# Optimization experiments

Measured on AMD Instinct MI355X. Metric: run time of the kernel, lower is better.

The kernel has to match this reference:

```python
import jax, jax.numpy as jnp
import numpy as np

D_MODEL = 1024
N_HEADS = 16
D_HEAD = 64


def setup_inputs() -> dict:
    key = jax.random.key(0)
    ks = jax.random.split(key, 9)
    B, T = 2, 2048
    s_in = 1.0 / np.sqrt(D_MODEL)
    s_o = 1.0 / np.sqrt(N_HEADS * D_HEAD)
    return {
        "x": jax.random.normal(ks[0], (B, T, D_MODEL), dtype=jnp.float32),
        "wq": jax.random.normal(ks[1], (D_MODEL, N_HEADS * D_HEAD), dtype=jnp.float32) * s_in,
        "bq": jax.random.normal(ks[2], (N_HEADS * D_HEAD,), dtype=jnp.float32) * 0.01,
        "wk": jax.random.normal(ks[3], (D_MODEL, N_HEADS * D_HEAD), dtype=jnp.float32) * s_in,
        "bk": jax.random.normal(ks[4], (N_HEADS * D_HEAD,), dtype=jnp.float32) * 0.01,
        "wv": jax.random.normal(ks[5], (D_MODEL, N_HEADS * D_HEAD), dtype=jnp.float32) * s_in,
        "bv": jax.random.normal(ks[6], (N_HEADS * D_HEAD,), dtype=jnp.float32) * 0.01,
        "wo": jax.random.normal(ks[7], (N_HEADS * D_HEAD, D_MODEL), dtype=jnp.float32) * s_o,
        "bo": jax.random.normal(ks[8], (D_MODEL,), dtype=jnp.float32) * 0.01,
    }


def reference(x, wq, bq, wk, bk, wv, bv, wo, bo):
    B, T, _ = x.shape
    H, Dh = N_HEADS, D_HEAD
    # projections -> [B, H, T, Dh]
    q = (x @ wq + bq).reshape(B, T, H, Dh).transpose(0, 2, 1, 3)
    k = (x @ wk + bk).reshape(B, T, H, Dh).transpose(0, 2, 1, 3)
    v = (x @ wv + bv).reshape(B, T, H, Dh).transpose(0, 2, 1, 3)
    scale = 1.0 / np.sqrt(Dh).astype(np.float32)
    attn = jnp.einsum("bhqd,bhkd->bhqk", q, k) * scale  # [B,H,T,T]
    causal = jnp.tril(jnp.ones((T, T), dtype=bool))
    attn = jnp.where(causal, attn, jnp.float32(-jnp.inf))
    attn = jax.nn.softmax(attn, axis=-1)
    out = jnp.einsum("bhqk,bhkd->bhqd", attn, v)  # [B,H,T,Dh]
    out = out.transpose(0, 2, 1, 3).reshape(B, T, H * Dh)
    return out @ wo + bo
```

## Files before the change

kernel.cpp:

```cpp
#include <hip/hip_runtime.h>
#include <math.h>

#define D_MODEL 1024
#define N_HEADS 16
#define D_HEAD  64
#define B_SZ    2
#define T_SEQ   2048

typedef short bf16x8 __attribute__((ext_vector_type(8)));
typedef short bf16x4 __attribute__((ext_vector_type(4)));
typedef float f32x4  __attribute__((ext_vector_type(4)));
typedef unsigned short us4 __attribute__((ext_vector_type(4)));

__device__ __forceinline__ unsigned short f2bf(float f) {
  union { float f; unsigned u; } v; v.f = f;
  unsigned r = v.u + 0x7FFFu + ((v.u >> 16) & 1u);
  return (unsigned short)(r >> 16);
}
__device__ __forceinline__ float bf2f(unsigned short s) {
  union { unsigned u; float f; } v; v.u = ((unsigned)s) << 16;
  return v.f;
}
__device__ __forceinline__ unsigned pack2_rtz(float lo, float hi) {
  union { float f; unsigned u; } a, b; a.f = hi; b.f = lo;
  return __builtin_amdgcn_perm(a.u, b.u, 0x07060302u);
}

__device__ __forceinline__ void async_copy16(const unsigned short* g, unsigned short* l) {
  __builtin_amdgcn_global_load_lds(
      (__attribute__((address_space(1))) void*)(g),
      (__attribute__((address_space(3))) void*)(l), 16, 0, 0);
}

__device__ __forceinline__ unsigned short* opart_ptr(
    unsigned short* wtd, unsigned short* xbd, int p) {
  const size_t off = (size_t)p * 2048;
  const size_t RA  = (size_t)3 * 1024 * 1024;
  return (off < RA) ? (wtd + off) : (xbd + (off - RA));
}

__global__ __launch_bounds__(256) void conv_all(
    const float* __restrict__ x,
    const float* __restrict__ wq, const float* __restrict__ wk,
    const float* __restrict__ wv, const float* __restrict__ wo,
    unsigned short* __restrict__ wt, unsigned short* __restrict__ xb)
{
  const int z = blockIdx.z;
  if (z < 4) {
    const float* W = (z == 0) ? wq : (z == 1) ? wk : (z == 2) ? wv : wo;
    unsigned short* O = wt + (size_t)z * D_MODEL * D_MODEL;
    __shared__ float t[32][33];
    const int tx = threadIdx.x & 31, ty = threadIdx.x >> 5;
    const int kb = blockIdx.x * 32, nb = blockIdx.y * 32;
    #pragma unroll
    for (int i = 0; i < 4; i++)
      t[ty + i * 8][tx] = W[(size_t)(kb + ty + i * 8) * D_MODEL + nb + tx];
    __syncthreads();
    #pragma unroll
    for (int i = 0; i < 4; i++)
      O[(size_t)(nb + ty + i * 8) * D_MODEL + kb + tx] = f2bf(t[tx][ty + i * 8]);
  } else {
    const int row = (z - 4) * 1024 + blockIdx.y * 32 + (threadIdx.x >> 3);
    const int col = blockIdx.x * 32 + (threadIdx.x & 7) * 4;
    float4 v = *(const float4*)&x[(size_t)row * D_MODEL + col];
    us4 o = { f2bf(v.x), f2bf(v.y), f2bf(v.z), f2bf(v.w) };
    *(us4*)&xb[(size_t)row * D_MODEL + col] = o;
  }
}

#define BKg 64
#define NTg (D_MODEL / BKg)
#define QSCALE 0.180336879f

__global__ __launch_bounds__(256) void qkv_gemm(
    const unsigned short* __restrict__ A, const unsigned short* __restrict__ Bt,
    const float* __restrict__ bq, const float* __restrict__ bk,
    const float* __restrict__ bv, unsigned short* __restrict__ qkv,
    unsigned short* __restrict__ vT)
{
  __shared__ unsigned short As[2][128 * BKg];

  const int tid  = threadIdx.x;
  const int wv   = tid >> 6;
  const int lane = tid & 63;
  const int lr   = lane & 15;
  const int quad = lane >> 4;
  const int wm   = wv >> 1;
  const int wn   = wv & 1;
  const int row0 = blockIdx.x * 128;
  const int col0 = blockIdx.y * 64;
  const int K = D_MODEL;

  const int mid = col0 >> 10;
  const float* bias = (mid == 0) ? bq : (mid == 1) ? bk : bv;

  f32x4 acc[8];
  #pragma unroll
  for (int i = 0; i < 8; i++) acc[i] = (f32x4){0.f, 0.f, 0.f, 0.f};

  auto stageA = [&](int buf, int k0) {
    #pragma unroll
    for (int it = 0; it < 4; it++) {
      const int gg = wv * 256 + it * 64 + lane;
      const int r  = gg >> 3;
      const int gc = ((gg & 7) ^ (r & 7)) * 8;
      async_copy16(A + (size_t)(row0 + r) * K + k0 + gc,
                   &As[buf][(size_t)(wv * 256 + it * 64) * 8]);
    }
  };

  const int wsel = (mid == 2) ? wn : wm;
  const unsigned short* Wp = Bt + (size_t)(col0 + wsel * 32 + lr) * K + quad * 8;

  auto loadW = [&](int k0, bf16x8 W[2][2]) {
    #pragma unroll
    for (int mi = 0; mi < 2; mi++)
      #pragma unroll
      for (int hf = 0; hf < 2; hf++)
        W[mi][hf] = *(const bf16x8*)&Wp[(size_t)mi * 16 * K + k0 + hf * 32];
  };

  bf16x8 Wc[2][2], Wn[2][2];
  loadW(0, Wc);
  stageA(0, 0);
  int cur = 0;

  const int xrow = (mid == 2) ? wm : wn;

  for (int t = 0; t < NTg; ++t) {
    __syncthreads();

    bf16x8 xF[4][2];
    #pragma unroll
    for (int hf = 0; hf < 2; hf++) {
      const int kc = ((hf * 4 + quad) ^ (lr & 7)) * 8;
      #pragma unroll
      for (int ni = 0; ni < 4; ni++)
        xF[ni][hf] = *(const bf16x8*)&As[cur][(xrow * 64 + ni * 16 + lr) * BKg + kc];
    }

    if (t + 1 < NTg) {
      stageA(cur ^ 1, (t + 1) * BKg);
      loadW((t + 1) * BKg, Wn);
    }

    if (mid == 2) {
      #pragma unroll
      for (int hf = 0; hf < 2; hf++)
        #pragma unroll
        for (int mi = 0; mi < 4; mi++)
          #pragma unroll
          for (int ni = 0; ni < 2; ni++)
            acc[mi * 2 + ni] = __builtin_amdgcn_mfma_f32_16x16x32_bf16(
                xF[mi][hf], Wc[ni][hf], acc[mi * 2 + ni], 0, 0, 0);
    } else {
      #pragma unroll
      for (int hf = 0; hf < 2; hf++)
        #pragma unroll
        for (int mi = 0; mi < 2; mi++)
          #pragma unroll
          for (int ni = 0; ni < 4; ni++)
            acc[mi * 4 + ni] = __builtin_amdgcn_mfma_f32_16x16x32_bf16(
                Wc[mi][hf], xF[ni][hf], acc[mi * 4 + ni], 0, 0, 0);
    }

    if (t + 1 < NTg) {
      #pragma unroll
      for (int mi = 0; mi < 2; mi++)
        #pragma unroll
        for (int hf = 0; hf < 2; hf++)
          Wc[mi][hf] = Wn[mi][hf];
    }
    cur ^= 1;
  }

  if (mid == 2) {
    #pragma unroll
    for (int ni = 0; ni < 2; ni++) {
      const int nn = (col0 & 1023) + wn * 32 + ni * 16 + lr;
      const float bv_ = bias[nn];
      const int h = nn >> 6, d = nn & 63;
      #pragma unroll
      for (int mi = 0; mi < 4; mi++) {
        const int t0_ = row0 + wm * 64 + mi * 16 + quad * 4;
        const int b = t0_ >> 11, tl = t0_ & 2047;
        us4 o;
        #pragma unroll
        for (int i = 0; i < 4; i++) o[i] = f2bf(acc[mi * 2 + ni][i] + bv_);
        *(us4*)&vT[((size_t)(b * N_HEADS + h) * D_HEAD + d) * T_SEQ + tl] = o;
      }
    }
  } else {
    unsigned short* dst = qkv + (size_t)mid * (4096u * 1024u);
    const float qs = (mid == 0) ? QSCALE : 1.0f;
    #pragma unroll
    for (int ni = 0; ni < 4; ni++) {
      const int t = row0 + wn * 64 + ni * 16 + lr;
      const int b = t >> 11, tl = t & 2047;
      #pragma unroll
      for (int mi = 0; mi < 2; mi++) {
        const int f = (col0 & 1023) + wm * 32 + mi * 16 + quad * 4;
        const int h = f >> 6, d = f & 63;
        const float4 b4 = *(const float4*)&bias[f];
        us4 o;
        o[0] = f2bf((acc[mi * 4 + ni][0] + b4.x) * qs);
        o[1] = f2bf((acc[mi * 4 + ni][1] + b4.y) * qs);
        o[2] = f2bf((acc[mi * 4 + ni][2] + b4.z) * qs);
        o[3] = f2bf((acc[mi * 4 + ni][3] + b4.w) * qs);
        *(us4*)&dst[((size_t)(b * N_HEADS + h) * T_SEQ + tl) * D_HEAD + d] = o;
      }
    }
  }
}

__global__ __launch_bounds__(256) void mfma_gemm(
    const unsigned short* __restrict__ A, const unsigned short* __restrict__ Bt,
    const float* __restrict__ bias, float* __restrict__ C,
    int M, int N, int K)
{
  __shared__ unsigned short As[2][128 * BKg];

  const int tid  = threadIdx.x;
  const int wv   = tid >> 6;
  const int lane = tid & 63;
  const int lr   = lane & 15;
  const int quad = lane >> 4;
  const int wm   = wv >> 1;
  const int wn   = wv & 1;
  const int row0 = blockIdx.x * 128;
  const int col0 = blockIdx.y * 64;

  f32x4 acc[4][2];
  #pragma unroll
  for (int mi = 0; mi < 4; mi++)
    #pragma unroll
    for (int ni = 0; ni < 2; ni++) acc[mi][ni] = (f32x4){0.f, 0.f, 0.f, 0.f};

  auto stageA = [&](int buf, int k0) {
    #pragma unroll
    for (int it = 0; it < 4; it++) {
      const int gg = wv * 256 + it * 64 + lane;
      const int r  = gg >> 3;
      const int gc = ((gg & 7) ^ (r & 7)) * 8;
      async_copy16(A + (size_t)(row0 + r) * K + k0 + gc,
                   &As[buf][(size_t)(wv * 256 + it * 64) * 8]);
    }
  };

  const unsigned short* Wp = Bt + (size_t)(col0 + wn * 32 + lr) * K + quad * 8;
  auto loadW = [&](int k0, bf16x8 W[2][2]) {
    #pragma unroll
    for (int ni = 0; ni < 2; ni++)
      #pragma unroll
      for (int hf = 0; hf < 2; hf++)
        W[ni][hf] = *(const bf16x8*)&Wp[(size_t)ni * 16 * K + k0 + hf * 32];
  };

  const int NT = K / BKg;
  bf16x8 Wc[2][2], Wn[2][2];
  loadW(0, Wc);
  stageA(0, 0);
  int cur = 0;

  for (int t = 0; t < NT; ++t) {
    __syncthreads();

    bf16x8 aF[4][2];
    #pragma unroll
    for (int hf = 0; hf < 2; hf++) {
      const int kc = ((hf * 4 + quad) ^ (lr & 7)) * 8;
      #pragma unroll
      for (int mi = 0; mi < 4; mi++)
        aF[mi][hf] = *(const bf16x8*)&As[cur][(wm * 64 + mi * 16 + lr) * BKg + kc];
    }

    if (t + 1 < NT) {
      stageA(cur ^ 1, (t + 1) * BKg);
      loadW((t + 1) * BKg, Wn);
    }

    #pragma unroll
    for (int hf = 0; hf < 2; hf++)
      #pragma unroll
      for (int mi = 0; mi < 4; mi++)
        #pragma unroll
        for (int ni = 0; ni < 2; ni++)
          acc[mi][ni] = __builtin_amdgcn_mfma_f32_16x16x32_bf16(
              aF[mi][hf], Wc[ni][hf], acc[mi][ni], 0, 0, 0);

    if (t + 1 < NT) {
      #pragma unroll
      for (int ni = 0; ni < 2; ni++)
        #pragma unroll
        for (int hf = 0; hf < 2; hf++)
          Wc[ni][hf] = Wn[ni][hf];
    }
    cur ^= 1;
  }

  #pragma unroll
  for (int ni = 0; ni < 2; ni++) {
    const int n = col0 + wn * 32 + ni * 16 + lr;
    const float bv = bias[n];
    #pragma unroll
    for (int mi = 0; mi < 4; mi++) {
      #pragma unroll
      for (int i = 0; i < 4; i++) {
        const int m = row0 + wm * 64 + mi * 16 + quad * 4 + i;
        C[(size_t)m * N + n] = acc[mi][ni][i] + bv;
      }
    }
  }
}

__global__ __launch_bounds__(256) void flash_part(
    const unsigned short* __restrict__ Q, const unsigned short* __restrict__ K,
    const unsigned short* __restrict__ Vt, unsigned short* __restrict__ Out,
    unsigned short* __restrict__ OpA, unsigned short* __restrict__ OpB,
    float* __restrict__ Lpart)
{
  const int bh = blockIdx.x;
  const int y  = blockIdx.y;
  int g, md;
  if (y < 28) { g = 15 - (y >> 1); md = 1 + (y & 1); }
  else        { g = 29 - y; md = 0; }

  const int b  = bh >> 4;
  const int h  = bh & 15;

  const unsigned short* Qb = Q  + (size_t)bh * T_SEQ * D_HEAD;
  const unsigned short* Kb = K  + (size_t)bh * T_SEQ * D_HEAD;
  const unsigned short* Vb = Vt + (size_t)bh * D_HEAD * T_SEQ;

  __shared__ __align__(16) unsigned short Ks[2][64 * 64];
  __shared__ __align__(16) unsigned short Vs[2][64 * 64];

  const int tid  = threadIdx.x;
  const int wv4  = tid >> 6;
  const int lane = tid & 63;
  const int lr   = lane & 15;
  const int quad = lane >> 4;

  const int qg      = 4 * g + wv4;
  const int q0      = qg * 32;
  const int my_full = 2 * g + 1 + (wv4 >> 1);
  const int tstart  = (md == 2) ? (g + 1) : 0;
  const int bend    = (md == 1) ? (g + 1) : (2 * g + 2);
  const int my_end  = (md == 1) ? (g + 1) : my_full;

  const int cbase = (tid & ~63);
  const int rr = tid >> 3;
  const int gcf = ((tid & 7) ^ (rr & 7)) * 8;
  const unsigned short* kp0 = Kb + (size_t)rr * D_HEAD + gcf;
  const unsigned short* vp0 = Vb + (size_t)rr * T_SEQ + gcf;

  auto stage = [&](int buf, int tile) {
    const unsigned short* kt = kp0 + (size_t)tile * (64 * D_HEAD);
    const unsigned short* vt = vp0 + (size_t)tile * 64;
    async_copy16(kt,                    &Ks[buf][(size_t)cbase * 8]);
    async_copy16(kt + 32 * D_HEAD,      &Ks[buf][(size_t)(256 + cbase) * 8]);
    async_copy16(vt,                    &Vs[buf][(size_t)cbase * 8]);
    async_copy16(vt + (size_t)32 * T_SEQ, &Vs[buf][(size_t)(256 + cbase) * 8]);
  };

  bf16x8 bQ[2][2];
  #pragma unroll
  for (int qb = 0; qb < 2; qb++)
    #pragma unroll
    for (int kh = 0; kh < 2; kh++)
      bQ[qb][kh] = *(const bf16x8*)&Qb[(size_t)(q0 + qb * 16 + lr) * D_HEAD + kh * 32 + quad * 8];

  f32x4 oacc[2][4];
  #pragma unroll
  for (int qb = 0; qb < 2; qb++)
    #pragma unroll
    for (int dt = 0; dt < 4; dt++) oacc[qb][dt] = (f32x4){0.f, 0.f, 0.f, 0.f};
  f32x4 lacc[2] = {(f32x4){0.f, 0.f, 0.f, 0.f}, (f32x4){0.f, 0.f, 0.f, 0.f}};

  const bf16x4 vONE = {(short)0x3F80, (short)0x3F80, (short)0x3F80, (short)0x3F80};

  int cur = 0;
  stage(0, tstart);

  for (int j = tstart; j < bend; j++) {
    __syncthreads();
    const bool act = (j < my_end);
    const unsigned short* KsB = &Ks[cur][0];
    const unsigned short* VsB = &Vs[cur][0];
    const int kv0 = j * 64;

    bf16x8 aK[4][2];
    bf16x4 aV[4][4];
    if (act) {
      #pragma unroll
      for (int nt = 0; nt < 4; nt++) {
        const int row = nt * 16 + lr;
        #pragma unroll
        for (int kh = 0; kh < 2; kh++) {
          const int sc = (kh * 4 + quad) ^ (row & 7);
          aK[nt][kh] = *(const bf16x8*)&KsB[row * 64 + sc * 8];
        }
      }
      #pragma unroll
      for (int dt = 0; dt < 4; dt++) {
        const int row = dt * 16 + lr;
        #pragma unroll
        for (int ks = 0; ks < 4; ks++) {
          const int sc = (ks * 2 + (quad >> 1)) ^ (row & 7);
          aV[dt][ks] = *(const bf16x4*)&VsB[row * 64 + sc * 8 + (quad & 1) * 4];
        }
      }
    }

    if (j + 1 < bend) stage(cur ^ 1, j + 1);

    if (act) {
      f32x4 sacc[2][4];
      __builtin_amdgcn_s_setprio(1);
      #pragma unroll
      for (int nt = 0; nt < 4; nt++) {
        #pragma unroll
        for (int qb = 0; qb < 2; qb++) {
          f32x4 c = (f32x4){0.f, 0.f, 0.f, 0.f};
          c = __builtin_amdgcn_mfma_f32_16x16x32_bf16(aK[nt][0], bQ[qb][0], c, 0, 0, 0);
          c = __builtin_amdgcn_mfma_f32_16x16x32_bf16(aK[nt][1], bQ[qb][1], c, 0, 0, 0);
          sacc[qb][nt] = c;
        }
      }
      __builtin_amdgcn_s_setprio(0);

      const bool diag = (j == my_full - 1);
      bf16x4 bP[2][4];
      #pragma unroll
      for (int qb = 0; qb < 2; qb++) {
        if (diag) {
          const int qcol = q0 + qb * 16 + lr;
          #pragma unroll
          for (int nt = 0; nt < 4; nt++)
            #pragma unroll
            for (int i = 0; i < 4; i++)
              if (kv0 + nt * 16 + quad * 4 + i > qcol) sacc[qb][nt][i] = -INFINITY;
        }
        #pragma unroll
        for (int nt = 0; nt < 4; nt++) {
          float p[4];
          #pragma unroll
          for (int i = 0; i < 4; i++)
            p[i] = __builtin_amdgcn_exp2f(sacc[qb][nt][i]);
          union { unsigned u[2]; bf16x4 v; } pk;
          pk.u[0] = pack2_rtz(p[0], p[1]);
          pk.u[1] = pack2_rtz(p[2], p[3]);
          bP[qb][nt] = pk.v;
        }
      }

      __builtin_amdgcn_s_setprio(1);
      #pragma unroll
      for (int ks = 0; ks < 4; ks++) {
        #pragma unroll
        for (int qb = 0; qb < 2; qb++) {
          lacc[qb] = __builtin_amdgcn_mfma_f32_16x16x16bf16_1k(
              vONE, bP[qb][ks], lacc[qb], 0, 0, 0);
          #pragma unroll
          for (int dt = 0; dt < 4; dt++)
            oacc[qb][dt] = __builtin_amdgcn_mfma_f32_16x16x16bf16_1k(
                aV[dt][ks], bP[qb][ks], oacc[qb][dt], 0, 0, 0);
        }
      }
      __builtin_amdgcn_s_setprio(0);
    }
    cur ^= 1;
  }

  float l_i[2] = {lacc[0][0], lacc[1][0]};

  if (md == 0) {
    #pragma unroll
    for (int qb = 0; qb < 2; qb++) {
      const float invl = __builtin_amdgcn_rcpf(l_i[qb]);
      const size_t orow = (size_t)(b * T_SEQ + q0 + qb * 16 + lr) * D_MODEL + h * D_HEAD;
      #pragma unroll
      for (int dt = 0; dt < 4; dt++) {
        us4 o;
        #pragma unroll
        for (int i = 0; i < 4; i++) o[i] = f2bf(oacc[qb][dt][i] * invl);
        *(us4*)&Out[orow + dt * 16 + quad * 4] = o;
      }
    }
  } else {
    const int s = md - 1;
    const int p = (bh * 56 + (qg - 8)) * 2 + s;
    unsigned short* Op = opart_ptr(OpA, OpB, p);
    if (quad == 0) {
      Lpart[(p * 2 + 0) * 16 + lr] = l_i[0];
      Lpart[(p * 2 + 1) * 16 + lr] = l_i[1];
    }
    #pragma unroll
    for (int qb = 0; qb < 2; qb++) {
      #pragma unroll
      for (int dt = 0; dt < 4; dt++) {
        us4 o;
        #pragma unroll
        for (int i = 0; i < 4; i++) o[i] = f2bf(oacc[qb][dt][i]);
        *(us4*)&Op[(size_t)(((qb * 4 + dt) * 64) + lane) * 4] = o;
      }
    }
  }
}

__global__ __launch_bounds__(64) void flash_reduce(
    unsigned short* __restrict__ OpA, unsigned short* __restrict__ OpB,
    const float* __restrict__ Lpart, unsigned short* __restrict__ Out)
{
  const int bh  = blockIdx.x;
  const int qgr = blockIdx.y;
  const int q0  = (8 + qgr) * 32;
  const int b   = bh >> 4;
  const int h   = bh & 15;
  const int lane = threadIdx.x;
  const int lr   = lane & 15;
  const int quad = lane >> 4;

  const int item = bh * 56 + qgr;
  const int p0 = item * 2, p1 = item * 2 + 1;
  const unsigned short* O0 = opart_ptr(OpA, OpB, p0);
  const unsigned short* O1 = opart_ptr(OpA, OpB, p1);

  #pragma unroll
  for (int qb = 0; qb < 2; qb++) {
    const float l0 = Lpart[(p0 * 2 + qb) * 16 + lr];
    const float l1 = Lpart[(p1 * 2 + qb) * 16 + lr];
    const float invL = __builtin_amdgcn_rcpf(l0 + l1);
    const size_t orow = (size_t)(b * T_SEQ + q0 + qb * 16 + lr) * D_MODEL + h * D_HEAD;
    #pragma unroll
    for (int dt = 0; dt < 4; dt++) {
      us4 o0 = *(const us4*)&O0[(size_t)(((qb * 4 + dt) * 64) + lane) * 4];
      us4 o1 = *(const us4*)&O1[(size_t)(((qb * 4 + dt) * 64) + lane) * 4];
      us4 o;
      #pragma unroll
      for (int i = 0; i < 4; i++)
        o[i] = f2bf((bf2f(o0[i]) + bf2f(o1[i])) * invL);
      *(us4*)&Out[orow + dt * 16 + quad * 4] = o;
    }
  }
}

extern "C" void kernel_launch(void* const* d_in, const int* in_sizes, int n_in,
                              void* d_out, int out_size, void* d_ws, size_t ws_size,
                              hipStream_t stream) {
  (void)in_sizes; (void)n_in; (void)out_size; (void)ws_size;

  const float* x  = (const float*)d_in[0];
  const float* wq = (const float*)d_in[1];
  const float* bq = (const float*)d_in[2];
  const float* wk = (const float*)d_in[3];
  const float* bk = (const float*)d_in[4];
  const float* wv = (const float*)d_in[5];
  const float* bv = (const float*)d_in[6];
  const float* wo = (const float*)d_in[7];
  const float* bo = (const float*)d_in[8];
  float* out = (float*)d_out;

  const int M = B_SZ * T_SEQ;
  const int N = D_MODEL;
  const int K = D_MODEL;
  const size_t MN = (size_t)M * N;
  const size_t WN = (size_t)N * N;

  unsigned short* wt    = (unsigned short*)d_ws;
  unsigned short* xb    = wt + 4 * WN;
  unsigned short* qkv   = xb + MN;
  unsigned short* qb    = qkv;
  unsigned short* kb    = qkv + MN;
  unsigned short* vT    = qkv + 2 * MN;
  unsigned short* attnb = vT + MN;
  float* Lpart = (float*)(attnb + MN);

  conv_all<<<dim3(32, 32, 8), dim3(256), 0, stream>>>(x, wq, wk, wv, wo, wt, xb);

  qkv_gemm<<<dim3(M / 128, 48), dim3(256), 0, stream>>>(xb, wt, bq, bk, bv, qkv, vT);

  flash_part<<<dim3(B_SZ * N_HEADS, 30), dim3(256), 0, stream>>>(
      qb, kb, vT, attnb, wt, xb, Lpart);
  flash_reduce<<<dim3(B_SZ * N_HEADS, 56), dim3(64), 0, stream>>>(
      wt, xb, Lpart, attnb);

  mfma_gemm<<<dim3(M / 128, N / 64), dim3(256), 0, stream>>>(attnb, wt + 3 * WN, bo, out, M, N, K);
}
```

Baseline: 217.3 us.

## Pre-swizzle bf16 weights into MFMA fragment order and ping-pong weight registers

The weight conversion kernel now writes bf16 weights in a fragment-blocked layout. Each lane's 16-byte MFMA operand is then contiguous with its neighbours, so the GEMM weight loads become fully coalesced lane*8 reads instead of strided row reads. The K loop in both GEMMs is unrolled by two, alternating the current and prefetch register buffers, which removes the per-iteration register copy. This adds indexing cost in the conversion kernel, whose stores are now scattered, and the two-step loop assumes an even tile count.

```diff
diff --git a/kernel.cpp b/kernel.cpp
--- a/kernel.cpp
+++ b/kernel.cpp
@@ -6,6 +6,7 @@
 #define D_HEAD  64
 #define B_SZ    2
 #define T_SEQ   2048
+#define WN_ELEMS (1024u * 1024u)
 
 typedef short bf16x8 __attribute__((ext_vector_type(8)));
 typedef short bf16x4 __attribute__((ext_vector_type(4)));
@@ -30,6 +31,12 @@
   __builtin_amdgcn_global_load_lds(
       (__attribute__((address_space(1))) void*)(g),
       (__attribute__((address_space(3))) void*)(l), 16, 0, 0);
+}
+
+__device__ __forceinline__ size_t widx(int n, int k) {
+  const int fb = n >> 5, mi = (n >> 4) & 1, lr = n & 15;
+  const int kt = k >> 6, hf = (k >> 5) & 1, quad = (k >> 3) & 3, e = k & 7;
+  return ((size_t)(fb * 16 + kt) * 4 + (mi * 2 + hf)) * 512 + (quad * 16 + lr) * 8 + e;
 }
 
 __device__ __forceinline__ unsigned short* opart_ptr(
@@ -48,7 +55,7 @@
   const int z = blockIdx.z;
   if (z < 4) {
     const float* W = (z == 0) ? wq : (z == 1) ? wk : (z == 2) ? wv : wo;
-    unsigned short* O = wt + (size_t)z * D_MODEL * D_MODEL;
+    unsigned short* O = wt + (size_t)z * WN_ELEMS;
     __shared__ float t[32][33];
     const int tx = threadIdx.x & 31, ty = threadIdx.x >> 5;
     const int kb = blockIdx.x * 32, nb = blockIdx.y * 32;
@@ -58,7 +65,7 @@
     __syncthreads();
     #pragma unroll
     for (int i = 0; i < 4; i++)
-      O[(size_t)(nb + ty + i * 8) * D_MODEL + kb + tx] = f2bf(t[tx][ty + i * 8]);
+      O[widx(nb + ty + i * 8, kb + tx)] = f2bf(t[tx][ty + i * 8]);
   } else {
     const int row = (z - 4) * 1024 + blockIdx.y * 32 + (threadIdx.x >> 3);
     const int col = blockIdx.x * 32 + (threadIdx.x & 7) * 4;
@@ -110,24 +117,26 @@
   };
 
   const int wsel = (mid == 2) ? wn : wm;
-  const unsigned short* Wp = Bt + (size_t)(col0 + wsel * 32 + lr) * K + quad * 8;
-
-  auto loadW = [&](int k0, bf16x8 W[2][2]) {
+  const int fb   = ((col0 & 1023) >> 5) + wsel;
+  const unsigned short* Wp =
+      Bt + (size_t)mid * WN_ELEMS + (size_t)fb * (16 * 2048) + lane * 8;
+
+  auto loadW = [&](int kt, bf16x8 (&W)[2][2]) {
     #pragma unroll
     for (int mi = 0; mi < 2; mi++)
       #pragma unroll
       for (int hf = 0; hf < 2; hf++)
-        W[mi][hf] = *(const bf16x8*)&Wp[(size_t)mi * 16 * K + k0 + hf * 32];
-  };
+        W[mi][hf] = *(const bf16x8*)&Wp[((size_t)kt * 4 + mi * 2 + hf) * 512];
+  };
+
+  const int xrow = (mid == 2) ? wm : wn;
 
   bf16x8 Wc[2][2], Wn[2][2];
   loadW(0, Wc);
   stageA(0, 0);
   int cur = 0;
 
-  const int xrow = (mid == 2) ? wm : wn;
-
-  for (int t = 0; t < NTg; ++t) {
+  auto kstep = [&](int t, bf16x8 (&Wuse)[2][2], bf16x8 (&Wpre)[2][2]) {
     __syncthreads();
 
     bf16x8 xF[4][2];
@@ -141,7 +150,7 @@
 
     if (t + 1 < NTg) {
       stageA(cur ^ 1, (t + 1) * BKg);
-      loadW((t + 1) * BKg, Wn);
+      loadW(t + 1, Wpre);
     }
 
     if (mid == 2) {
@@ -152,7 +161,7 @@
           #pragma unroll
           for (int ni = 0; ni < 2; ni++)
             acc[mi * 2 + ni] = __builtin_amdgcn_mfma_f32_16x16x32_bf16(
-                xF[mi][hf], Wc[ni][hf], acc[mi * 2 + ni], 0, 0, 0);
+                xF[mi][hf], Wuse[ni][hf], acc[mi * 2 + ni], 0, 0, 0);
     } else {
       #pragma unroll
       for (int hf = 0; hf < 2; hf++)
@@ -161,17 +170,15 @@
           #pragma unroll
           for (int ni = 0; ni < 4; ni++)
             acc[mi * 4 + ni] = __builtin_amdgcn_mfma_f32_16x16x32_bf16(
-                Wc[mi][hf], xF[ni][hf], acc[mi * 4 + ni], 0, 0, 0);
-    }
-
-    if (t + 1 < NTg) {
-      #pragma unroll
-      for (int mi = 0; mi < 2; mi++)
-        #pragma unroll
-        for (int hf = 0; hf < 2; hf++)
-          Wc[mi][hf] = Wn[mi][hf];
+                Wuse[mi][hf], xF[ni][hf], acc[mi * 4 + ni], 0, 0, 0);
     }
     cur ^= 1;
+  };
+
+  #pragma unroll 1
+  for (int t = 0; t < NTg; t += 2) {
+    kstep(t,     Wc, Wn);
+    kstep(t + 1, Wn, Wc);
   }
 
   if (mid == 2) {
@@ -247,13 +254,14 @@
     }
   };
 
-  const unsigned short* Wp = Bt + (size_t)(col0 + wn * 32 + lr) * K + quad * 8;
-  auto loadW = [&](int k0, bf16x8 W[2][2]) {
+  const int fb = (col0 >> 5) + wn;
+  const unsigned short* Wp = Bt + (size_t)fb * (16 * 2048) + lane * 8;
+  auto loadW = [&](int kt, bf16x8 (&W)[2][2]) {
     #pragma unroll
     for (int ni = 0; ni < 2; ni++)
       #pragma unroll
       for (int hf = 0; hf < 2; hf++)
-        W[ni][hf] = *(const bf16x8*)&Wp[(size_t)ni * 16 * K + k0 + hf * 32];
+        W[ni][hf] = *(const bf16x8*)&Wp[((size_t)kt * 4 + ni * 2 + hf) * 512];
   };
 
   const int NT = K / BKg;
@@ -262,7 +270,7 @@
   stageA(0, 0);
   int cur = 0;
 
-  for (int t = 0; t < NT; ++t) {
+  auto kstep = [&](int t, bf16x8 (&Wuse)[2][2], bf16x8 (&Wpre)[2][2]) {
     __syncthreads();
 
     bf16x8 aF[4][2];
@@ -276,7 +284,7 @@
 
     if (t + 1 < NT) {
       stageA(cur ^ 1, (t + 1) * BKg);
-      loadW((t + 1) * BKg, Wn);
+      loadW(t + 1, Wpre);
     }
 
     #pragma unroll
@@ -286,16 +294,14 @@
         #pragma unroll
         for (int ni = 0; ni < 2; ni++)
           acc[mi][ni] = __builtin_amdgcn_mfma_f32_16x16x32_bf16(
-              aF[mi][hf], Wc[ni][hf], acc[mi][ni], 0, 0, 0);
-
-    if (t + 1 < NT) {
-      #pragma unroll
-      for (int ni = 0; ni < 2; ni++)
-        #pragma unroll
-        for (int hf = 0; hf < 2; hf++)
-          Wc[ni][hf] = Wn[ni][hf];
-    }
+              aF[mi][hf], Wuse[ni][hf], acc[mi][ni], 0, 0, 0);
     cur ^= 1;
+  };
+
+  #pragma unroll 1
+  for (int t = 0; t < NT; t += 2) {
+    kstep(t,     Wc, Wn);
+    kstep(t + 1, Wn, Wc);
   }
 
   #pragma unroll
```

Result: faster. 188.9 us (-13.1%).
